# Performance work log

Hardware: AMD Instinct MI355X
Metric: run time of the kernel (lower is better)

The kernel has to match this reference:

```python
import jax, jax.numpy as jnp
import numpy as np

D_MODEL = 1024
N_HEADS = 16
N_GROUPS = 4
HEAD_DIM = D_MODEL // N_HEADS          # 64
KV_HEADS = N_HEADS // N_GROUPS         # 4
D_KV = D_MODEL // N_GROUPS             # 256
B, S = 2, 2048


def setup_inputs() -> dict:
    key = jax.random.key(0)
    ks = jax.random.split(key, 10)
    sd = 1.0 / np.sqrt(D_MODEL)
    x = jax.random.normal(ks[0], (B, S, D_MODEL), dtype=jnp.float32)
    # causal mask: True means masked (matches masked_fill semantics)
    mask = jnp.triu(jnp.ones((S, S), dtype=bool), k=1)
    Wq = jax.random.normal(ks[1], (D_MODEL, D_MODEL), jnp.float32) * sd
    bq = jnp.zeros((D_MODEL,), jnp.float32)
    Wk = jax.random.normal(ks[2], (D_MODEL, D_KV), jnp.float32) * sd
    bk = jnp.zeros((D_KV,), jnp.float32)
    Wv = jax.random.normal(ks[3], (D_MODEL, D_KV), jnp.float32) * sd
    bv = jnp.zeros((D_KV,), jnp.float32)
    Wo = jax.random.normal(ks[4], (D_MODEL, D_MODEL), jnp.float32) * sd
    bo = jnp.zeros((D_MODEL,), jnp.float32)
    return {"x": x, "Wq": Wq, "bq": bq, "Wk": Wk, "bk": bk,
            "Wv": Wv, "bv": bv, "Wo": Wo, "bo": bo, "mask": mask}


def reference(x, Wq, bq, Wk, bk, Wv, bv, Wo, bo, mask):
    b, s, _ = x.shape
    scale = 1.0 / jnp.sqrt(jnp.float32(HEAD_DIM))
    # Q: [b, n_heads, s, head_dim]
    Q = (x @ Wq + bq).reshape(b, s, N_HEADS, HEAD_DIM).transpose(0, 2, 1, 3)
    # K, V: [b, kv_heads, s, head_dim]
    K = (x @ Wk + bk).reshape(b, s, KV_HEADS, HEAD_DIM).transpose(0, 2, 1, 3)
    V = (x @ Wv + bv).reshape(b, s, KV_HEADS, HEAD_DIM).transpose(0, 2, 1, 3)
    # expand: each kv head repeated n_groups consecutive times -> [b, n_heads, s, hd]
    K = jnp.repeat(K, N_GROUPS, axis=1)
    V = jnp.repeat(V, N_GROUPS, axis=1)
    scores = jnp.einsum('bhqd,bhkd->bhqk', Q, K) * scale
    scores = jnp.where(mask, -jnp.inf, scores)
    attn = jax.nn.softmax(scores, axis=-1)
    out = jnp.einsum('bhqk,bhkd->bhqd', attn, V)          # [b, h, s, hd]
    out = out.transpose(0, 2, 1, 3).reshape(b, s, D_MODEL)
    return out @ Wo + bo
```

## Files before the change

### kernel.cpp

```cpp
#include <hip/hip_runtime.h>
#include <hip/hip_bf16.h>
#include <stdint.h>

#define D_MODEL 1024
#define N_HEADS 16
#define HEAD_DIM 64
#define KV_HEADS 4
#define BATCH 2
#define SEQ 2048
#define MROWS (BATCH * SEQ)
#define NQKV 1536
#define QKV_K_OFF 1024
#define QKV_V_OFF 1280

typedef __attribute__((ext_vector_type(8))) short bf16x8;
typedef __attribute__((ext_vector_type(4))) short short4v;
typedef __attribute__((ext_vector_type(4))) float f32x4;

__device__ __forceinline__ short f2bf(float f) {
    union { float f; unsigned u; } c; c.f = f;
    unsigned u = c.u + 0x7fffu + ((c.u >> 16) & 1u);
    return (short)(u >> 16);
}

__global__ __launch_bounds__(256) void convert_bf16_kernel(
    const float* __restrict__ in, short* __restrict__ out, int n4)
{
    int i = blockIdx.x * 256 + threadIdx.x;
    if (i < n4) {
        float4 v = ((const float4*)in)[i];
        short4v o;
        o.x = f2bf(v.x); o.y = f2bf(v.y); o.z = f2bf(v.z); o.w = f2bf(v.w);
        ((short4v*)out)[i] = o;
    }
}

__global__ __launch_bounds__(256) void transpose_w_kernel(
    const float* __restrict__ in, int N, short* __restrict__ out)
{
    __shared__ short Ts[64][68];
    const int n0 = blockIdx.x * 64, k0 = blockIdx.y * 64;
    const int t = threadIdx.x;
    const int r = t >> 4, c4 = (t & 15) * 4;
    #pragma unroll
    for (int i = 0; i < 4; ++i) {
        int k = r + i * 16;
        float4 v = *(const float4*)(in + (size_t)(k0 + k) * N + n0 + c4);
        Ts[c4 + 0][k] = f2bf(v.x);
        Ts[c4 + 1][k] = f2bf(v.y);
        Ts[c4 + 2][k] = f2bf(v.z);
        Ts[c4 + 3][k] = f2bf(v.w);
    }
    __syncthreads();
    #pragma unroll
    for (int i = 0; i < 4; ++i) {
        int n = r + i * 16;
        short4v o = *(short4v*)&Ts[n][c4];
        *(short4v*)(out + (size_t)(n0 + n) * 1024 + k0 + c4) = o;
    }
}

__global__ __launch_bounds__(256) void bias_concat_kernel(
    const float* __restrict__ bq, const float* __restrict__ bk,
    const float* __restrict__ bv, float* __restrict__ bcat)
{
    int n = blockIdx.x * 256 + threadIdx.x;
    if (n < NQKV)
        bcat[n] = n < 1024 ? bq[n] : (n < 1280 ? bk[n - 1024] : bv[n - 1280]);
}

template <bool BF16_OUT>
__global__ __launch_bounds__(256) void gemm_kernel(
    const short* __restrict__ A, const short* __restrict__ Bt,
    const float* __restrict__ bias, void* __restrict__ Cv, int N)
{
    __shared__ short As[128 * 64];
    __shared__ short Bs[128 * 64];
    const int t = threadIdx.x;
    const int l = t & 63;
    const int w = t >> 6;
    const int bm = blockIdx.y * 128, bn = blockIdx.x * 128;
    const int wr = (w >> 1) * 64, wc = (w & 1) * 64;
    const int lr = l & 15, lg = l >> 4;

    f32x4 acc[4][4] = {};
    bf16x8 ra[4], rb[4];

    #pragma unroll
    for (int i = 0; i < 4; ++i) {
        int u = t + 256 * i, row = u >> 3, s = u & 7;
        ra[i] = *(const bf16x8*)(A  + (size_t)(bm + row) * 1024 + s * 8);
        rb[i] = *(const bf16x8*)(Bt + (size_t)(bn + row) * 1024 + s * 8);
    }

    for (int k0 = 0; k0 < 1024; k0 += 64) {
        __syncthreads();
        #pragma unroll
        for (int i = 0; i < 4; ++i) {
            int u = t + 256 * i, row = u >> 3, s = u & 7;
            int sd = s ^ (row & 7);
            *(bf16x8*)(&As[row * 64 + sd * 8]) = ra[i];
            *(bf16x8*)(&Bs[row * 64 + sd * 8]) = rb[i];
        }
        if (k0 + 64 < 1024) {
            #pragma unroll
            for (int i = 0; i < 4; ++i) {
                int u = t + 256 * i, row = u >> 3, s = u & 7;
                ra[i] = *(const bf16x8*)(A  + (size_t)(bm + row) * 1024 + k0 + 64 + s * 8);
                rb[i] = *(const bf16x8*)(Bt + (size_t)(bn + row) * 1024 + k0 + 64 + s * 8);
            }
        }
        __syncthreads();
        #pragma unroll
        for (int tt = 0; tt < 2; ++tt) {
            bf16x8 af[4], bfr[4];
            #pragma unroll
            for (int mi = 0; mi < 4; ++mi) {
                int m = wr + mi * 16 + lr;
                af[mi]  = *(const bf16x8*)(&As[m * 64 + ((tt * 4 + lg) ^ (m & 7)) * 8]);
                int n = wc + mi * 16 + lr;
                bfr[mi] = *(const bf16x8*)(&Bs[n * 64 + ((tt * 4 + lg) ^ (n & 7)) * 8]);
            }
            #pragma unroll
            for (int mi = 0; mi < 4; ++mi)
                #pragma unroll
                for (int ni = 0; ni < 4; ++ni)
                    acc[mi][ni] = __builtin_amdgcn_mfma_f32_16x16x32_bf16(
                        af[mi], bfr[ni], acc[mi][ni], 0, 0, 0);
        }
    }

    #pragma unroll
    for (int ni = 0; ni < 4; ++ni) {
        int n = bn + wc + ni * 16 + lr;
        float bv = bias[n];
        #pragma unroll
        for (int mi = 0; mi < 4; ++mi) {
            #pragma unroll
            for (int r = 0; r < 4; ++r) {
                int m = bm + wr + mi * 16 + lg * 4 + r;
                float v = acc[mi][ni][r] + bv;
                if constexpr (BF16_OUT)
                    ((short*)Cv)[(size_t)m * N + n] = f2bf(v);
                else
                    ((float*)Cv)[(size_t)m * N + n] = v;
            }
        }
    }
}

__global__ __launch_bounds__(256) void attn_kernel(
    const short* __restrict__ QKV, short* __restrict__ Aout)
{
    __shared__ short Qs[64 * 64];
    __shared__ short Ks[64 * 64];
    __shared__ short Vt[64 * 64];
    __shared__ short Ps[4 * 16 * 64];

    const int t = threadIdx.x, l = t & 63, w = t >> 6;
    const int h = blockIdx.y, b = blockIdx.z;
    const int kvh = h >> 2;
    const int lr = l & 15, lg = l >> 4;
    const float SCL = 0.125f * 1.44269504f;

    const size_t baseQ = (size_t)(b * SEQ) * NQKV + h * 64;
    const size_t baseK = (size_t)(b * SEQ) * NQKV + QKV_K_OFF + kvh * 64;
    const size_t baseV = (size_t)(b * SEQ) * NQKV + QKV_V_OFF + kvh * 64;

    for (int pi = 0; pi < 2; ++pi) {
        const int qb = pi ? (31 - (int)blockIdx.x) : (int)blockIdx.x;
        const int q0 = qb * 64;
        __syncthreads();

        #pragma unroll
        for (int i = 0; i < 2; ++i) {
            int u = t + 256 * i, row = u >> 3, s = u & 7;
            bf16x8 v = *(const bf16x8*)(QKV + baseQ + (size_t)(q0 + row) * NQKV + s * 8);
            *(bf16x8*)(&Qs[row * 64 + (s ^ (row & 7)) * 8]) = v;
        }
        bf16x8 rk[2], rv[2];
        #pragma unroll
        for (int i = 0; i < 2; ++i) {
            int u = t + 256 * i, row = u >> 3, s = u & 7;
            rk[i] = *(const bf16x8*)(QKV + baseK + (size_t)row * NQKV + s * 8);
        }
        #pragma unroll
        for (int c = 0; c < 2; ++c) {
            int d0 = (w * 2 + c) * 8;
            rv[c] = *(const bf16x8*)(QKV + baseV + (size_t)l * NQKV + d0);
        }
        __syncthreads();

        bf16x8 qf[2];
        #pragma unroll
        for (int tt = 0; tt < 2; ++tt) {
            int q = w * 16 + lr;
            qf[tt] = *(const bf16x8*)(&Qs[q * 64 + ((tt * 4 + lg) ^ (q & 7)) * 8]);
        }

        float m_i[4], l_i[4];
        f32x4 o[4];
        #pragma unroll
        for (int r = 0; r < 4; ++r) { m_i[r] = -INFINITY; l_i[r] = 0.f; }
        #pragma unroll
        for (int ni = 0; ni < 4; ++ni) o[ni] = (f32x4){0.f, 0.f, 0.f, 0.f};

        for (int kb = 0; kb <= qb; ++kb) {
            __syncthreads();
            #pragma unroll
            for (int i = 0; i < 2; ++i) {
                int u = t + 256 * i, row = u >> 3, s = u & 7;
                *(bf16x8*)(&Ks[row * 64 + (s ^ (row & 7)) * 8]) = rk[i];
            }
            #pragma unroll
            for (int c = 0; c < 2; ++c) {
                int d0 = (w * 2 + c) * 8;
                #pragma unroll
                for (int m = 0; m < 8; ++m) {
                    int d = d0 + m;
                    Vt[d * 64 + (((l >> 3) ^ (d & 7)) * 8) + (l & 7)] = rv[c][m];
                }
            }
            if (kb < qb) {
                int kn = (kb + 1) * 64;
                #pragma unroll
                for (int i = 0; i < 2; ++i) {
                    int u = t + 256 * i, row = u >> 3, s = u & 7;
                    rk[i] = *(const bf16x8*)(QKV + baseK + (size_t)(kn + row) * NQKV + s * 8);
                }
                #pragma unroll
                for (int c = 0; c < 2; ++c) {
                    int d0 = (w * 2 + c) * 8;
                    rv[c] = *(const bf16x8*)(QKV + baseV + (size_t)(kn + l) * NQKV + d0);
                }
            }
            __syncthreads();

            f32x4 sf[4] = {};
            #pragma unroll
            for (int tt = 0; tt < 2; ++tt) {
                #pragma unroll
                for (int ni = 0; ni < 4; ++ni) {
                    int kc = ni * 16 + lr;
                    bf16x8 kf = *(const bf16x8*)(&Ks[kc * 64 + ((tt * 4 + lg) ^ (kc & 7)) * 8]);
                    sf[ni] = __builtin_amdgcn_mfma_f32_16x16x32_bf16(qf[tt], kf, sf[ni], 0, 0, 0);
                }
            }

            float z[4][4];
            #pragma unroll
            for (int ni = 0; ni < 4; ++ni) {
                #pragma unroll
                for (int r = 0; r < 4; ++r) {
                    float v = sf[ni][r] * SCL;
                    if (kb == qb && (ni * 16 + lr) > (w * 16 + lg * 4 + r))
                        v = -INFINITY;
                    z[ni][r] = v;
                }
            }

            #pragma unroll
            for (int r = 0; r < 4; ++r) {
                float rm = fmaxf(fmaxf(z[0][r], z[1][r]), fmaxf(z[2][r], z[3][r]));
                rm = fmaxf(rm, __shfl_xor(rm, 1));
                rm = fmaxf(rm, __shfl_xor(rm, 2));
                rm = fmaxf(rm, __shfl_xor(rm, 4));
                rm = fmaxf(rm, __shfl_xor(rm, 8));
                float mnew = fmaxf(m_i[r], rm);
                float corr = exp2f(m_i[r] - mnew);
                float rs = 0.f;
                int qr = lg * 4 + r;
                #pragma unroll
                for (int ni = 0; ni < 4; ++ni) {
                    float p = exp2f(z[ni][r] - mnew);
                    rs += p;
                    int k = ni * 16 + lr;
                    Ps[w * 1024 + qr * 64 + (((k >> 3) ^ (qr & 7)) * 8) + (k & 7)] = f2bf(p);
                }
                rs += __shfl_xor(rs, 1);
                rs += __shfl_xor(rs, 2);
                rs += __shfl_xor(rs, 4);
                rs += __shfl_xor(rs, 8);
                l_i[r] = l_i[r] * corr + rs;
                m_i[r] = mnew;
                #pragma unroll
                for (int ni = 0; ni < 4; ++ni) o[ni][r] *= corr;
            }

            #pragma unroll
            for (int tt = 0; tt < 2; ++tt) {
                bf16x8 pf = *(const bf16x8*)(&Ps[w * 1024 + lr * 64 + ((tt * 4 + lg) ^ (lr & 7)) * 8]);
                #pragma unroll
                for (int ni = 0; ni < 4; ++ni) {
                    int d = ni * 16 + lr;
                    bf16x8 vf = *(const bf16x8*)(&Vt[d * 64 + ((tt * 4 + lg) ^ (d & 7)) * 8]);
                    o[ni] = __builtin_amdgcn_mfma_f32_16x16x32_bf16(pf, vf, o[ni], 0, 0, 0);
                }
            }
        }

        #pragma unroll
        for (int r = 0; r < 4; ++r) {
            float inv = 1.0f / l_i[r];
            int q = q0 + w * 16 + lg * 4 + r;
            #pragma unroll
            for (int ni = 0; ni < 4; ++ni) {
                Aout[(size_t)(b * SEQ + q) * D_MODEL + h * 64 + ni * 16 + lr] =
                    f2bf(o[ni][r] * inv);
            }
        }
    }
}

extern "C" void kernel_launch(void* const* d_in, const int* in_sizes, int n_in,
                              void* d_out, int out_size, void* d_ws, size_t ws_size,
                              hipStream_t stream) {
    const float* x  = (const float*)d_in[0];
    const float* Wq = (const float*)d_in[1];
    const float* bq = (const float*)d_in[2];
    const float* Wk = (const float*)d_in[3];
    const float* bk = (const float*)d_in[4];
    const float* Wv = (const float*)d_in[5];
    const float* bv = (const float*)d_in[6];
    const float* Wo = (const float*)d_in[7];
    const float* bo = (const float*)d_in[8];
    float* out = (float*)d_out;

    short* xb    = (short*)d_ws;
    short* BtQKV = xb    + (size_t)MROWS * D_MODEL;
    short* WoT   = BtQKV + (size_t)NQKV * 1024;
    short* QKV   = WoT   + (size_t)1024 * 1024;
    short* Abuf  = QKV   + (size_t)MROWS * NQKV;
    float* bcat  = (float*)(Abuf + (size_t)MROWS * D_MODEL);

    dim3 blk(256);
    convert_bf16_kernel<<<dim3(MROWS * D_MODEL / 4 / 256), blk, 0, stream>>>(
        x, xb, MROWS * D_MODEL / 4);
    transpose_w_kernel<<<dim3(16, 16), blk, 0, stream>>>(Wq, 1024, BtQKV);
    transpose_w_kernel<<<dim3(4, 16),  blk, 0, stream>>>(Wk, 256,  BtQKV + (size_t)1024 * 1024);
    transpose_w_kernel<<<dim3(4, 16),  blk, 0, stream>>>(Wv, 256,  BtQKV + (size_t)1280 * 1024);
    transpose_w_kernel<<<dim3(16, 16), blk, 0, stream>>>(Wo, 1024, WoT);
    bias_concat_kernel<<<dim3(6), blk, 0, stream>>>(bq, bk, bv, bcat);
    gemm_kernel<true><<<dim3(NQKV / 128, MROWS / 128), blk, 0, stream>>>(
        xb, BtQKV, bcat, QKV, NQKV);
    attn_kernel<<<dim3(16, N_HEADS, BATCH), blk, 0, stream>>>(QKV, Abuf);
    gemm_kernel<false><<<dim3(D_MODEL / 128, MROWS / 128), blk, 0, stream>>>(
        Abuf, WoT, bo, out, D_MODEL);
}
```

Before: 222.2 us.

## Use direct global-to-LDS loads in GEMM and transpose attention MFMA layout

The GEMM now loads A/B tiles directly into LDS with global_load_lds instead of staging through registers, dropping the register prefetch and the LDS swizzle. The attention kernel swaps MFMA operand order so each lane owns a whole query row. That turns the per-row shuffle reductions into two cross-group shuffles, packs P stores, and vectorises output writes. It also launches one block per query tile instead of pairing tiles, and raises wave priority around the MFMA sections. Risks are LDS bank conflicts from the unswizzled GEMM tiles, no more overlap of the next tile's loads with compute, and load imbalance across causal blocks.

```diff
diff --git a/kernel.cpp b/kernel.cpp
--- a/kernel.cpp
+++ b/kernel.cpp
@@ -22,6 +22,17 @@
     unsigned u = c.u + 0x7fffu + ((c.u >> 16) & 1u);
     return (short)(u >> 16);
 }
+__device__ __forceinline__ unsigned pack_bf16(float a, float b) {
+    return ((unsigned)(unsigned short)f2bf(a)) |
+           (((unsigned)(unsigned short)f2bf(b)) << 16);
+}
+
+__device__ __forceinline__ void gload_lds16(const short* g, short* l) {
+    __builtin_amdgcn_global_load_lds(
+        (const __attribute__((address_space(1))) unsigned int*)g,
+        (__attribute__((address_space(3))) unsigned int*)l,
+        16, 0, 0);
+}
 
 __global__ __launch_bounds__(256) void convert_bf16_kernel(
     const float* __restrict__ in, short* __restrict__ out, int n4)
@@ -84,31 +95,14 @@
     const int lr = l & 15, lg = l >> 4;
 
     f32x4 acc[4][4] = {};
-    bf16x8 ra[4], rb[4];
-
-    #pragma unroll
-    for (int i = 0; i < 4; ++i) {
-        int u = t + 256 * i, row = u >> 3, s = u & 7;
-        ra[i] = *(const bf16x8*)(A  + (size_t)(bm + row) * 1024 + s * 8);
-        rb[i] = *(const bf16x8*)(Bt + (size_t)(bn + row) * 1024 + s * 8);
-    }
 
     for (int k0 = 0; k0 < 1024; k0 += 64) {
         __syncthreads();
         #pragma unroll
         for (int i = 0; i < 4; ++i) {
             int u = t + 256 * i, row = u >> 3, s = u & 7;
-            int sd = s ^ (row & 7);
-            *(bf16x8*)(&As[row * 64 + sd * 8]) = ra[i];
-            *(bf16x8*)(&Bs[row * 64 + sd * 8]) = rb[i];
-        }
-        if (k0 + 64 < 1024) {
-            #pragma unroll
-            for (int i = 0; i < 4; ++i) {
-                int u = t + 256 * i, row = u >> 3, s = u & 7;
-                ra[i] = *(const bf16x8*)(A  + (size_t)(bm + row) * 1024 + k0 + 64 + s * 8);
-                rb[i] = *(const bf16x8*)(Bt + (size_t)(bn + row) * 1024 + k0 + 64 + s * 8);
-            }
+            gload_lds16(A  + (size_t)(bm + row) * 1024 + k0 + s * 8, &As[u * 8]);
+            gload_lds16(Bt + (size_t)(bn + row) * 1024 + k0 + s * 8, &Bs[u * 8]);
         }
         __syncthreads();
         #pragma unroll
@@ -116,10 +110,8 @@
             bf16x8 af[4], bfr[4];
             #pragma unroll
             for (int mi = 0; mi < 4; ++mi) {
-                int m = wr + mi * 16 + lr;
-                af[mi]  = *(const bf16x8*)(&As[m * 64 + ((tt * 4 + lg) ^ (m & 7)) * 8]);
-                int n = wc + mi * 16 + lr;
-                bfr[mi] = *(const bf16x8*)(&Bs[n * 64 + ((tt * 4 + lg) ^ (n & 7)) * 8]);
+                af[mi]  = *(const bf16x8*)(&As[(wr + mi * 16 + lr) * 64 + (tt * 4 + lg) * 8]);
+                bfr[mi] = *(const bf16x8*)(&Bs[(wc + mi * 16 + lr) * 64 + (tt * 4 + lg) * 8]);
             }
             #pragma unroll
             for (int mi = 0; mi < 4; ++mi)
@@ -167,148 +159,159 @@
     const size_t baseK = (size_t)(b * SEQ) * NQKV + QKV_K_OFF + kvh * 64;
     const size_t baseV = (size_t)(b * SEQ) * NQKV + QKV_V_OFF + kvh * 64;
 
-    for (int pi = 0; pi < 2; ++pi) {
-        const int qb = pi ? (31 - (int)blockIdx.x) : (int)blockIdx.x;
-        const int q0 = qb * 64;
+    const int qb = blockIdx.x;
+    const int q0 = qb * 64;
+
+    #pragma unroll
+    for (int i = 0; i < 2; ++i) {
+        int u = t + 256 * i, row = u >> 3, s = u & 7;
+        bf16x8 v = *(const bf16x8*)(QKV + baseQ + (size_t)(q0 + row) * NQKV + s * 8);
+        *(bf16x8*)(&Qs[row * 64 + (s ^ (row & 7)) * 8]) = v;
+    }
+    bf16x8 rk[2], rv[2];
+    #pragma unroll
+    for (int i = 0; i < 2; ++i) {
+        int u = t + 256 * i, row = u >> 3, s = u & 7;
+        rk[i] = *(const bf16x8*)(QKV + baseK + (size_t)row * NQKV + s * 8);
+    }
+    #pragma unroll
+    for (int c = 0; c < 2; ++c) {
+        int d0 = (w * 2 + c) * 8;
+        rv[c] = *(const bf16x8*)(QKV + baseV + (size_t)l * NQKV + d0);
+    }
+    __syncthreads();
+
+    bf16x8 qf[2];
+    #pragma unroll
+    for (int tt = 0; tt < 2; ++tt) {
+        int q = w * 16 + lr;
+        qf[tt] = *(const bf16x8*)(&Qs[q * 64 + ((tt * 4 + lg) ^ (lr & 7)) * 8]);
+    }
+
+    float m_i = -INFINITY, l_i = 0.f;
+    f32x4 o[4];
+    #pragma unroll
+    for (int ni = 0; ni < 4; ++ni) o[ni] = (f32x4){0.f, 0.f, 0.f, 0.f};
+
+    const int qg = q0 + w * 16 + lr;
+
+    for (int kb = 0; kb <= qb; ++kb) {
         __syncthreads();
-
         #pragma unroll
         for (int i = 0; i < 2; ++i) {
             int u = t + 256 * i, row = u >> 3, s = u & 7;
-            bf16x8 v = *(const bf16x8*)(QKV + baseQ + (size_t)(q0 + row) * NQKV + s * 8);
-            *(bf16x8*)(&Qs[row * 64 + (s ^ (row & 7)) * 8]) = v;
-        }
-        bf16x8 rk[2], rv[2];
-        #pragma unroll
-        for (int i = 0; i < 2; ++i) {
-            int u = t + 256 * i, row = u >> 3, s = u & 7;
-            rk[i] = *(const bf16x8*)(QKV + baseK + (size_t)row * NQKV + s * 8);
+            *(bf16x8*)(&Ks[row * 64 + (s ^ (row & 7)) * 8]) = rk[i];
         }
         #pragma unroll
         for (int c = 0; c < 2; ++c) {
             int d0 = (w * 2 + c) * 8;
-            rv[c] = *(const bf16x8*)(QKV + baseV + (size_t)l * NQKV + d0);
-        }
-        __syncthreads();
-
-        bf16x8 qf[2];
-        #pragma unroll
-        for (int tt = 0; tt < 2; ++tt) {
-            int q = w * 16 + lr;
-            qf[tt] = *(const bf16x8*)(&Qs[q * 64 + ((tt * 4 + lg) ^ (q & 7)) * 8]);
-        }
-
-        float m_i[4], l_i[4];
-        f32x4 o[4];
-        #pragma unroll
-        for (int r = 0; r < 4; ++r) { m_i[r] = -INFINITY; l_i[r] = 0.f; }
-        #pragma unroll
-        for (int ni = 0; ni < 4; ++ni) o[ni] = (f32x4){0.f, 0.f, 0.f, 0.f};
-
-        for (int kb = 0; kb <= qb; ++kb) {
-            __syncthreads();
+            #pragma unroll
+            for (int m = 0; m < 8; ++m) {
+                int d = d0 + m;
+                Vt[d * 64 + (((l >> 3) ^ (d & 7)) * 8) + (l & 7)] = rv[c][m];
+            }
+        }
+        if (kb < qb) {
+            int kn = (kb + 1) * 64;
             #pragma unroll
             for (int i = 0; i < 2; ++i) {
                 int u = t + 256 * i, row = u >> 3, s = u & 7;
-                *(bf16x8*)(&Ks[row * 64 + (s ^ (row & 7)) * 8]) = rk[i];
+                rk[i] = *(const bf16x8*)(QKV + baseK + (size_t)(kn + row) * NQKV + s * 8);
             }
             #pragma unroll
             for (int c = 0; c < 2; ++c) {
                 int d0 = (w * 2 + c) * 8;
+                rv[c] = *(const bf16x8*)(QKV + baseV + (size_t)(kn + l) * NQKV + d0);
+            }
+        }
+        __syncthreads();
+
+        f32x4 sf[4];
+        #pragma unroll
+        for (int ni = 0; ni < 4; ++ni) sf[ni] = (f32x4){0.f, 0.f, 0.f, 0.f};
+        __builtin_amdgcn_s_setprio(1);
+        #pragma unroll
+        for (int tt = 0; tt < 2; ++tt) {
+            #pragma unroll
+            for (int ni = 0; ni < 4; ++ni) {
+                int kvr = ni * 16 + lr;
+                bf16x8 kf = *(const bf16x8*)(&Ks[kvr * 64 + ((tt * 4 + lg) ^ (lr & 7)) * 8]);
+                sf[ni] = __builtin_amdgcn_mfma_f32_16x16x32_bf16(kf, qf[tt], sf[ni], 0, 0, 0);
+            }
+        }
+        __builtin_amdgcn_s_setprio(0);
+
+        float p[4][4];
+        #pragma unroll
+        for (int ni = 0; ni < 4; ++ni)
+            #pragma unroll
+            for (int r = 0; r < 4; ++r)
+                p[ni][r] = sf[ni][r] * SCL;
+        if (kb == qb) {
+            #pragma unroll
+            for (int ni = 0; ni < 4; ++ni)
                 #pragma unroll
-                for (int m = 0; m < 8; ++m) {
-                    int d = d0 + m;
-                    Vt[d * 64 + (((l >> 3) ^ (d & 7)) * 8) + (l & 7)] = rv[c][m];
-                }
-            }
-            if (kb < qb) {
-                int kn = (kb + 1) * 64;
-                #pragma unroll
-                for (int i = 0; i < 2; ++i) {
-                    int u = t + 256 * i, row = u >> 3, s = u & 7;
-                    rk[i] = *(const bf16x8*)(QKV + baseK + (size_t)(kn + row) * NQKV + s * 8);
-                }
-                #pragma unroll
-                for (int c = 0; c < 2; ++c) {
-                    int d0 = (w * 2 + c) * 8;
-                    rv[c] = *(const bf16x8*)(QKV + baseV + (size_t)(kn + l) * NQKV + d0);
-                }
-            }
-            __syncthreads();
-
-            f32x4 sf[4] = {};
-            #pragma unroll
-            for (int tt = 0; tt < 2; ++tt) {
-                #pragma unroll
-                for (int ni = 0; ni < 4; ++ni) {
-                    int kc = ni * 16 + lr;
-                    bf16x8 kf = *(const bf16x8*)(&Ks[kc * 64 + ((tt * 4 + lg) ^ (kc & 7)) * 8]);
-                    sf[ni] = __builtin_amdgcn_mfma_f32_16x16x32_bf16(qf[tt], kf, sf[ni], 0, 0, 0);
-                }
-            }
-
-            float z[4][4];
+                for (int r = 0; r < 4; ++r)
+                    if (kb * 64 + ni * 16 + lg * 4 + r > qg)
+                        p[ni][r] = -INFINITY;
+        }
+
+        float rm = fmaxf(fmaxf(fmaxf(p[0][0], p[0][1]), fmaxf(p[0][2], p[0][3])),
+                         fmaxf(fmaxf(p[1][0], p[1][1]), fmaxf(p[1][2], p[1][3])));
+        rm = fmaxf(rm, fmaxf(fmaxf(fmaxf(p[2][0], p[2][1]), fmaxf(p[2][2], p[2][3])),
+                             fmaxf(fmaxf(p[3][0], p[3][1]), fmaxf(p[3][2], p[3][3]))));
+        rm = fmaxf(rm, __shfl_xor(rm, 16));
+        rm = fmaxf(rm, __shfl_xor(rm, 32));
+        float mnew = fmaxf(m_i, rm);
+        float corr = exp2f(m_i - mnew);
+        float rs = 0.f;
+        #pragma unroll
+        for (int ni = 0; ni < 4; ++ni)
+            #pragma unroll
+            for (int r = 0; r < 4; ++r) {
+                float pv = exp2f(p[ni][r] - mnew);
+                p[ni][r] = pv;
+                rs += pv;
+            }
+        rs += __shfl_xor(rs, 16);
+        rs += __shfl_xor(rs, 32);
+        l_i = l_i * corr + rs;
+        m_i = mnew;
+        #pragma unroll
+        for (int ni = 0; ni < 4; ++ni) o[ni] *= corr;
+
+        #pragma unroll
+        for (int ni = 0; ni < 4; ++ni) {
+            int slot = (ni * 2 + (lg >> 1)) ^ (lr & 7);
+            short* bp = &Ps[w * 1024 + lr * 64 + slot * 8 + (lg & 1) * 4];
+            *(unsigned*)(bp)     = pack_bf16(p[ni][0], p[ni][1]);
+            *(unsigned*)(bp + 2) = pack_bf16(p[ni][2], p[ni][3]);
+        }
+
+        __builtin_amdgcn_s_setprio(1);
+        #pragma unroll
+        for (int tt = 0; tt < 2; ++tt) {
+            bf16x8 pf = *(const bf16x8*)(&Ps[w * 1024 + lr * 64 + ((tt * 4 + lg) ^ (lr & 7)) * 8]);
             #pragma unroll
             for (int ni = 0; ni < 4; ++ni) {
-                #pragma unroll
-                for (int r = 0; r < 4; ++r) {
-                    float v = sf[ni][r] * SCL;
-                    if (kb == qb && (ni * 16 + lr) > (w * 16 + lg * 4 + r))
-                        v = -INFINITY;
-                    z[ni][r] = v;
-                }
-            }
-
-            #pragma unroll
-            for (int r = 0; r < 4; ++r) {
-                float rm = fmaxf(fmaxf(z[0][r], z[1][r]), fmaxf(z[2][r], z[3][r]));
-                rm = fmaxf(rm, __shfl_xor(rm, 1));
-                rm = fmaxf(rm, __shfl_xor(rm, 2));
-                rm = fmaxf(rm, __shfl_xor(rm, 4));
-                rm = fmaxf(rm, __shfl_xor(rm, 8));
-                float mnew = fmaxf(m_i[r], rm);
-                float corr = exp2f(m_i[r] - mnew);
-                float rs = 0.f;
-                int qr = lg * 4 + r;
-                #pragma unroll
-                for (int ni = 0; ni < 4; ++ni) {
-                    float p = exp2f(z[ni][r] - mnew);
-                    rs += p;
-                    int k = ni * 16 + lr;
-                    Ps[w * 1024 + qr * 64 + (((k >> 3) ^ (qr & 7)) * 8) + (k & 7)] = f2bf(p);
-                }
-                rs += __shfl_xor(rs, 1);
-                rs += __shfl_xor(rs, 2);
-                rs += __shfl_xor(rs, 4);
-                rs += __shfl_xor(rs, 8);
-                l_i[r] = l_i[r] * corr + rs;
-                m_i[r] = mnew;
-                #pragma unroll
-                for (int ni = 0; ni < 4; ++ni) o[ni][r] *= corr;
-            }
-
-            #pragma unroll
-            for (int tt = 0; tt < 2; ++tt) {
-                bf16x8 pf = *(const bf16x8*)(&Ps[w * 1024 + lr * 64 + ((tt * 4 + lg) ^ (lr & 7)) * 8]);
-                #pragma unroll
-                for (int ni = 0; ni < 4; ++ni) {
-                    int d = ni * 16 + lr;
-                    bf16x8 vf = *(const bf16x8*)(&Vt[d * 64 + ((tt * 4 + lg) ^ (d & 7)) * 8]);
-                    o[ni] = __builtin_amdgcn_mfma_f32_16x16x32_bf16(pf, vf, o[ni], 0, 0, 0);
-                }
-            }
-        }
-
-        #pragma unroll
-        for (int r = 0; r < 4; ++r) {
-            float inv = 1.0f / l_i[r];
-            int q = q0 + w * 16 + lg * 4 + r;
-            #pragma unroll
-            for (int ni = 0; ni < 4; ++ni) {
-                Aout[(size_t)(b * SEQ + q) * D_MODEL + h * 64 + ni * 16 + lr] =
-                    f2bf(o[ni][r] * inv);
-            }
-        }
+                int d = ni * 16 + lr;
+                bf16x8 vf = *(const bf16x8*)(&Vt[d * 64 + ((tt * 4 + lg) ^ (lr & 7)) * 8]);
+                o[ni] = __builtin_amdgcn_mfma_f32_16x16x32_bf16(vf, pf, o[ni], 0, 0, 0);
+            }
+        }
+        __builtin_amdgcn_s_setprio(0);
+    }
+
+    float inv = 1.0f / l_i;
+    const size_t orow = (size_t)(b * SEQ + qg) * D_MODEL + h * 64;
+    #pragma unroll
+    for (int ni = 0; ni < 4; ++ni) {
+        short4v ov;
+        ov.x = f2bf(o[ni][0] * inv);
+        ov.y = f2bf(o[ni][1] * inv);
+        ov.z = f2bf(o[ni][2] * inv);
+        ov.w = f2bf(o[ni][3] * inv);
+        *(short4v*)(Aout + orow + ni * 16 + lg * 4) = ov;
     }
 }
 
@@ -343,7 +346,7 @@
     bias_concat_kernel<<<dim3(6), blk, 0, stream>>>(bq, bk, bv, bcat);
     gemm_kernel<true><<<dim3(NQKV / 128, MROWS / 128), blk, 0, stream>>>(
         xb, BtQKV, bcat, QKV, NQKV);
-    attn_kernel<<<dim3(16, N_HEADS, BATCH), blk, 0, stream>>>(QKV, Abuf);
+    attn_kernel<<<dim3(32, N_HEADS, BATCH), blk, 0, stream>>>(QKV, Abuf);
     gemm_kernel<false><<<dim3(D_MODEL / 128, MROWS / 128), blk, 0, stream>>>(
         Abuf, WoT, bo, out, D_MODEL);
 }
```

Result: slower. 264.0 us (+18.8%).
